# Kernel optimization log

Measured on AMD Instinct MI355X. Metric: run time of the kernel, lower is better.

The kernel has to match this reference:

```python
import jax, jax.numpy as jnp
import numpy as np

N = 50000      # nodes
E = 800000     # edges (before self-loops)
IN = 64        # in_dim
C = 64         # hidden_dim (per-head out channels)
H = 4          # heads
NEG_SLOPE = 0.2


def setup_inputs() -> dict:
    key = jax.random.key(0)
    ks = jax.random.split(key, 9)
    x = jax.random.normal(ks[0], (N, IN), jnp.float32)
    edge_index = jax.random.randint(ks[1], (2, E), 0, N)
    edge_attr = jax.random.uniform(ks[2], (E, 1), jnp.float32)
    s_in = 1.0 / np.sqrt(IN)
    s_c = 1.0 / np.sqrt(C)
    W = jax.random.normal(ks[3], (IN, H * C), jnp.float32) * s_in
    att_src = jax.random.normal(ks[4], (H, C), jnp.float32) * s_c
    att_dst = jax.random.normal(ks[5], (H, C), jnp.float32) * s_c
    lin_edge_w = jax.random.normal(ks[6], (1, H * C), jnp.float32)
    att_edge = jax.random.normal(ks[7], (H, C), jnp.float32) * s_c
    bias = jnp.zeros((C,), jnp.float32)
    return dict(x=x, edge_index=edge_index, edge_attr=edge_attr, W=W,
                att_src=att_src, att_dst=att_dst, lin_edge_w=lin_edge_w,
                att_edge=att_edge, bias=bias)


def reference(x, edge_index, edge_attr, W, att_src, att_dst, lin_edge_w, att_edge, bias):
    n = x.shape[0]
    # add self-loops (PyG default add_self_loops=True, fill_value='mean')
    loop = jnp.arange(n)
    src = jnp.concatenate([edge_index[0], loop])          # [E+N]
    dst = jnp.concatenate([edge_index[1], loop])          # [E+N]
    ea = jnp.concatenate([edge_attr,
                          jnp.full((n, 1), edge_attr.mean(), edge_attr.dtype)], axis=0)
    # node transform: [N, H, C]
    h = (x @ W).reshape(n, H, C)
    a_src = jnp.einsum('nhc,hc->nh', h, att_src)          # [N, H]
    a_dst = jnp.einsum('nhc,hc->nh', h, att_dst)          # [N, H]
    eh = (ea @ lin_edge_w).reshape(-1, H, C)              # [E+N, H, C]
    a_edge = jnp.einsum('ehc,hc->eh', eh, att_edge)       # [E+N, H]
    # per-edge attention logit
    alpha = a_src[src] + a_dst[dst] + a_edge              # [E+N, H]
    alpha = jax.nn.leaky_relu(alpha, NEG_SLOPE)
    # segment softmax over edges grouped by destination node
    amax = jax.ops.segment_max(alpha, dst, num_segments=n)
    alpha = jnp.exp(alpha - amax[dst])
    asum = jax.ops.segment_sum(alpha, dst, num_segments=n)
    alpha = alpha / (asum[dst] + 1e-16)                   # [E+N, H]
    # weighted message + scatter-add aggregation
    msg = h[src] * alpha[..., None]                       # [E+N, H, C]
    out = jax.ops.segment_sum(msg, dst, num_segments=n)   # [N, H, C]
    out = out.mean(axis=1) + bias                         # concat=False -> head mean
    # ReLU + residual
    return jax.nn.relu(out) + x
```

## Files before the change

### kernel.cpp

```cpp
#include <hip/hip_runtime.h>
#include <hip/hip_fp16.h>
#include <math.h>

#define H 4
#define C 64
#define HC 256
#define NEG 0.2f
#define BKT 128
#define BSH 7
#define TILE 2048
#define CSEG 32
#define MAXCR 31
#define MAXREC 63
#define XPAD 72
#define G1 512
#define NBMAX 392

typedef __attribute__((ext_vector_type(8))) _Float16 half8;
typedef __attribute__((ext_vector_type(4))) float f32x4;
typedef float f32x2 __attribute__((vector_size(8)));

__global__ __launch_bounds__(256) void phase1_kernel(
    const float* __restrict__ x, const float* __restrict__ W,
    const float* __restrict__ att_src, const float* __restrict__ att_dst,
    const int* __restrict__ ei, const float* __restrict__ edge_attr,
    unsigned char* __restrict__ h, float* __restrict__ a_src, float* __restrict__ a_dst,
    unsigned* __restrict__ arena, float* __restrict__ mean_acc,
    int Nn, int Ee, int ntile, int nbkt) {
    __shared__ __align__(16) char smem[NBMAX * CSEG * 4 + 1024];
    int t = threadIdx.x;
    if ((int)blockIdx.x < G1) {
        _Float16* xs = (_Float16*)smem;
        int w = t >> 6, lane = t & 63, quad = lane >> 4, c16 = lane & 15;
        half8 bf[4][2];
#pragma unroll
        for (int nt = 0; nt < 4; ++nt)
#pragma unroll
            for (int kh = 0; kh < 2; ++kh)
#pragma unroll
                for (int j = 0; j < 8; ++j)
                    bf[nt][kh][j] = (_Float16)W[(kh * 32 + quad * 8 + j) * HC +
                                                w * 64 + nt * 16 + c16];
        float ats[4], atd[4];
#pragma unroll
        for (int nt = 0; nt < 4; ++nt) {
            ats[nt] = att_src[w * 64 + nt * 16 + c16];
            atd[nt] = att_dst[w * 64 + nt * 16 + c16];
        }
        unsigned* h32 = (unsigned*)h;

        int nT = (Nn + 15) >> 4;
        for (int mt = blockIdx.x; mt < nT; mt += G1) {
            __syncthreads();
            {
                int row = t >> 4, col4 = (t & 15) * 4;
                int node = mt * 16 + row;
                float4 v = make_float4(0.f, 0.f, 0.f, 0.f);
                if (node < Nn) v = *(const float4*)(x + (size_t)node * 64 + col4);
                _Float16* dst = xs + row * XPAD + col4;
                dst[0] = (_Float16)v.x; dst[1] = (_Float16)v.y;
                dst[2] = (_Float16)v.z; dst[3] = (_Float16)v.w;
            }
            __syncthreads();
            half8 a0 = *(const half8*)(xs + c16 * XPAD + quad * 8);
            half8 a1 = *(const half8*)(xs + c16 * XPAD + 32 + quad * 8);
            f32x4 d[4];
#pragma unroll
            for (int nt = 0; nt < 4; ++nt) {
                f32x4 acc = {0.f, 0.f, 0.f, 0.f};
                acc = __builtin_amdgcn_mfma_f32_16x16x32_f16(a0, bf[nt][0], acc, 0, 0, 0);
                acc = __builtin_amdgcn_mfma_f32_16x16x32_f16(a1, bf[nt][1], acc, 0, 0, 0);
                d[nt] = acc;
            }
#pragma unroll
            for (int reg = 0; reg < 4; ++reg) {
                int node = mt * 16 + quad * 4 + reg;
                float ps = 0.f, pd = 0.f;
#pragma unroll
                for (int nt = 0; nt < 4; ++nt) {
                    ps += d[nt][reg] * ats[nt];
                    pd += d[nt][reg] * atd[nt];
                }
                ps += __shfl_xor(ps, 1); pd += __shfl_xor(pd, 1);
                ps += __shfl_xor(ps, 2); pd += __shfl_xor(pd, 2);
                ps += __shfl_xor(ps, 4); pd += __shfl_xor(pd, 4);
                ps += __shfl_xor(ps, 8); pd += __shfl_xor(pd, 8);
                if (node < Nn) {
                    if (c16 == 0) {
                        a_src[node * 4 + w] = ps;
                        a_dst[node * 4 + w] = pd;
                    }
                    int v = __builtin_amdgcn_cvt_pk_fp8_f32(d[0][reg], d[1][reg], 0, false);
                    v = __builtin_amdgcn_cvt_pk_fp8_f32(d[2][reg], d[3][reg], v, true);
                    h32[(size_t)node * 64 + w * 16 + c16] = (unsigned)v;
                }
            }
        }
    } else {
        unsigned* img = (unsigned*)smem;
        float* red = (float*)(smem + NBMAX * CSEG * 4);
        int tile = (int)blockIdx.x - G1;
        for (int c = t; c < nbkt; c += 256) img[c * CSEG] = 0;
        __syncthreads();
        int e0 = tile * TILE;
        float s = 0.f;
#pragma unroll 4
        for (int k = 0; k < TILE / 256; ++k) {
            int i = e0 + k * 256 + t;
            if (i < Ee) {
                int src = ei[i];
                int dst = ei[Ee + i];
                float ea = edge_attr[i];
                s += ea;
                unsigned q = (unsigned)(ea * 511.f + 0.5f);
                int b = dst >> BSH;
                unsigned r = atomicAdd(&img[b * CSEG], 1u);
                if (r < MAXCR)
                    img[b * CSEG + 1 + r] =
                        ((unsigned)src << 16) | (q << 7) | (unsigned)(dst & (BKT - 1));
            }
        }
        __syncthreads();
        for (int j = t; j < nbkt * CSEG; j += 256) {
            unsigned v = img[j];
            if ((j & (CSEG - 1)) == 0) v = v < (unsigned)MAXCR ? v : (unsigned)MAXCR;
            arena[((size_t)(j >> 5) * ntile + tile) * CSEG + (j & (CSEG - 1))] = v;
        }
        red[t] = s;
        __syncthreads();
        for (int o = 128; o; o >>= 1) {
            if (t < o) red[t] += red[t + o];
            __syncthreads();
        }
        if (t == 0) atomicAdd(mean_acc, red[0]);
    }
}

__global__ __launch_bounds__(512) void aggregate_kernel(
    const unsigned* __restrict__ arena,
    const float* __restrict__ a_src, const float* __restrict__ a_dst,
    const float* __restrict__ lin_edge_w, const float* __restrict__ att_edge,
    const float* __restrict__ mean_acc, const unsigned char* __restrict__ h,
    const float* __restrict__ bias, const float* __restrict__ x,
    float* __restrict__ out, int Nn, int ntile, float invE) {
    __shared__ unsigned rows[BKT * 64 + 64];
    __shared__ unsigned rcnt[BKT];
    __shared__ unsigned short cellc[NBMAX];
    int t = threadIdx.x;
    int b = blockIdx.x;
    int lane = t & 63, w = t >> 6;

    if (t < BKT) rcnt[t] = 0;
    size_t base = (size_t)b * ntile * CSEG;
    for (int c = t; c < ntile; c += 512) {
        unsigned v = arena[base + (size_t)c * CSEG];
        cellc[c] = (unsigned short)(v < (unsigned)MAXCR ? v : (unsigned)MAXCR);
    }
    __syncthreads();
    int tot = ntile * CSEG;
    for (int j = t; j < tot; j += 512) {
        int slot = j & (CSEG - 1);
        if (slot >= 1 && slot <= (int)cellc[j >> 5]) {
            unsigned rec = arena[base + j];
            unsigned dl = rec & 127u;
            unsigned r = atomicAdd(&rcnt[dl], 1u);
            if (r < MAXREC) rows[dl * 64 + 1 + r] = rec;
        }
    }
    __syncthreads();
    if (t < BKT) rows[t * 64] = rcnt[t] < (unsigned)MAXREC ? rcnt[t] : (unsigned)MAXREC;
    __syncthreads();

    int head = lane >> 4, sub = lane & 15;
    float kp = 0.f;
#pragma unroll
    for (int j = 0; j < 4; ++j) {
        int c = sub * 4 + j;
        kp += lin_edge_w[head * C + c] * att_edge[head * C + c];
    }
    kp += __shfl_xor(kp, 1);
    kp += __shfl_xor(kp, 2);
    kp += __shfl_xor(kp, 4);
    kp += __shfl_xor(kp, 8);
    float K = kp;
    float mean = mean_acc[0] * invE;
    const unsigned* h8 = (const unsigned*)h;
    const float DEQ = 1.0f / 511.f;
    int hb = lane & 48;

    for (int i = 0; i < BKT / 8; ++i) {
        int nl = w * (BKT / 8) + i;
        int n = b * BKT + nl;
        if (n >= Nn) break;
        unsigned deg = rows[nl * 64];
        unsigned rec = rows[nl * 64 + 1 + lane];
        unsigned sv = h8[(size_t)n * 64 + lane];
        float ad = a_dst[n * 4 + head];
        float asn = a_src[n * 4 + head];

        float wk0, wk1, wk2, wk3;
        {
            float wtmp[4];
#pragma unroll
            for (int k2 = 0; k2 < 4; ++k2) {
                int e = sub + 16 * k2;
                unsigned re = (unsigned)__shfl((int)rec, e);
                int se = (e < (int)deg) ? (int)(re >> 16) : 0;
                float lg = a_src[se * 4 + head] + ad +
                           (float)((re >> 7) & 511u) * DEQ * K;
                lg = lg > 0.f ? lg : NEG * lg;
                wtmp[k2] = (e < (int)deg) ? __expf(lg) : 0.f;
            }
            wk0 = wtmp[0]; wk1 = wtmp[1]; wk2 = wtmp[2]; wk3 = wtmp[3];
        }
        float sw = (wk0 + wk1) + (wk2 + wk3);
        sw += __shfl_xor(sw, 1);
        sw += __shfl_xor(sw, 2);
        sw += __shfl_xor(sw, 4);
        sw += __shfl_xor(sw, 8);

        float ls = asn + ad + mean * K;
        ls = ls > 0.f ? ls : NEG * ls;
        float wsl = __expf(ls);
        f32x2 s01 = __builtin_amdgcn_cvt_pk_f32_fp8((int)sv, false);
        f32x2 s23 = __builtin_amdgcn_cvt_pk_f32_fp8((int)sv, true);
        float4 acc = make_float4(wsl * s01[0], wsl * s01[1], wsl * s23[0], wsl * s23[1]);
        float swgt = sw + wsl;

        for (int g = 0; g < (int)deg; g += 8) {
            int cnt = (int)deg - g;
            if (cnt > 8) cnt = 8;
            unsigned hv0 = 0, hv1 = 0, hv2 = 0, hv3 = 0,
                     hv4 = 0, hv5 = 0, hv6 = 0, hv7 = 0;
#define GATH(u, dst)                                                          \
            if (u < cnt) {                                                    \
                unsigned r = (unsigned)__builtin_amdgcn_readlane((int)rec, g + u); \
                dst = h8[(size_t)(r >> 16) * 64 + lane];                      \
            }
            GATH(0, hv0) GATH(1, hv1) GATH(2, hv2) GATH(3, hv3)
            GATH(4, hv4) GATH(5, hv5) GATH(6, hv6) GATH(7, hv7)
#undef GATH
#define CONS(u, src)                                                          \
            if (u < cnt) {                                                    \
                int e = g + u;                                                \
                int k2 = e >> 4;                                              \
                float wsrc = (k2 == 0) ? wk0 : (k2 == 1) ? wk1                \
                             : (k2 == 2) ? wk2 : wk3;                         \
                float wg = __shfl(wsrc, hb | (e & 15));                       \
                f32x2 f01 = __builtin_amdgcn_cvt_pk_f32_fp8((int)src, false); \
                f32x2 f23 = __builtin_amdgcn_cvt_pk_f32_fp8((int)src, true);  \
                acc.x += wg * f01[0]; acc.y += wg * f01[1];                   \
                acc.z += wg * f23[0]; acc.w += wg * f23[1];                   \
            }
            CONS(0, hv0) CONS(1, hv1) CONS(2, hv2) CONS(3, hv3)
            CONS(4, hv4) CONS(5, hv5) CONS(6, hv6) CONS(7, hv7)
#undef CONS
        }

        float inv = 1.f / (swgt + 1e-16f);
        acc.x *= inv; acc.y *= inv; acc.z *= inv; acc.w *= inv;

        acc.x += __shfl_xor(acc.x, 16);
        acc.y += __shfl_xor(acc.y, 16);
        acc.z += __shfl_xor(acc.z, 16);
        acc.w += __shfl_xor(acc.w, 16);
        acc.x += __shfl_xor(acc.x, 32);
        acc.y += __shfl_xor(acc.y, 32);
        acc.z += __shfl_xor(acc.z, 32);
        acc.w += __shfl_xor(acc.w, 32);
        if (lane < 16) {
            float b0 = bias[lane], b1 = bias[16 + lane];
            float b2 = bias[32 + lane], b3 = bias[48 + lane];
            const float* xr = x + (size_t)n * 64 + lane;
            float x0 = xr[0], x1 = xr[16], x2 = xr[32], x3 = xr[48];
            float* orow = out + (size_t)n * 64 + lane;
            orow[0]  = fmaxf(acc.x * 0.25f + b0, 0.f) + x0;
            orow[16] = fmaxf(acc.y * 0.25f + b1, 0.f) + x1;
            orow[32] = fmaxf(acc.z * 0.25f + b2, 0.f) + x2;
            orow[48] = fmaxf(acc.w * 0.25f + b3, 0.f) + x3;
        }
    }
}

extern "C" void kernel_launch(void* const* d_in, const int* in_sizes, int n_in,
                              void* d_out, int out_size, void* d_ws, size_t ws_size,
                              hipStream_t stream) {
    const float* x = (const float*)d_in[0];
    const int* ei = (const int*)d_in[1];
    const float* edge_attr = (const float*)d_in[2];
    const float* W = (const float*)d_in[3];
    const float* att_src = (const float*)d_in[4];
    const float* att_dst = (const float*)d_in[5];
    const float* lin_edge_w = (const float*)d_in[6];
    const float* att_edge = (const float*)d_in[7];
    const float* bias = (const float*)d_in[8];
    float* out = (float*)d_out;
    int Nn = in_sizes[0] / 64;
    int Ee = in_sizes[1] / 2;
    int nbkt = (Nn + BKT - 1) >> BSH;
    int ntile = (Ee + TILE - 1) / TILE;

    char* p = (char*)d_ws;
    size_t off = 0;
    auto alloc = [&](size_t bytes) -> char* {
        char* r = p + off;
        off += (bytes + 255) & ~(size_t)255;
        return r;
    };
    float* mean_acc = (float*)alloc(256);
    size_t zero_bytes = off;
    unsigned* arena = (unsigned*)alloc((size_t)nbkt * ntile * CSEG * 4);
    unsigned char* h = (unsigned char*)alloc((size_t)Nn * HC);
    float* a_src = (float*)alloc((size_t)Nn * H * 4);
    float* a_dst = (float*)alloc((size_t)Nn * H * 4);
    (void)ws_size;

    hipMemsetAsync(d_ws, 0, zero_bytes, stream);
    phase1_kernel<<<G1 + ntile, 256, 0, stream>>>(x, W, att_src, att_dst,
                                                  ei, edge_attr, h, a_src, a_dst,
                                                  arena, mean_acc,
                                                  Nn, Ee, ntile, nbkt);
    aggregate_kernel<<<nbkt, 512, 0, stream>>>(arena, a_src, a_dst,
                                               lin_edge_w, att_edge, mean_acc,
                                               h, bias, x, out, Nn, ntile,
                                               1.0f / (float)Ee);
}
```

Baseline: 175.4 us.

## Split bucket compaction from aggregation into separate per-node-wave kernel

Splits the fused aggregate kernel into two. A bucket kernel compacts arena records into per-node rows in global memory, and a new aggregate kernel assigns one wave per node across many small blocks. The aim is finer-grained parallelism and better latency hiding than the old layout, where a 512-thread block per 128-node bucket looped over 16 nodes per wave behind a large shared-memory footprint. In exchange it adds an extra launch and a global round trip for the compacted edge rows.

```diff
diff --git a/kernel.cpp b/kernel.cpp
--- a/kernel.cpp
+++ b/kernel.cpp
@@ -136,29 +136,22 @@
     }
 }
 
-__global__ __launch_bounds__(512) void aggregate_kernel(
-    const unsigned* __restrict__ arena,
-    const float* __restrict__ a_src, const float* __restrict__ a_dst,
-    const float* __restrict__ lin_edge_w, const float* __restrict__ att_edge,
-    const float* __restrict__ mean_acc, const unsigned char* __restrict__ h,
-    const float* __restrict__ bias, const float* __restrict__ x,
-    float* __restrict__ out, int Nn, int ntile, float invE) {
-    __shared__ unsigned rows[BKT * 64 + 64];
+__global__ __launch_bounds__(256) void bucket_kernel(
+    const unsigned* __restrict__ arena, unsigned* __restrict__ edges,
+    int ntile, int nbkt) {
+    __shared__ unsigned rows[BKT * 64];
     __shared__ unsigned rcnt[BKT];
     __shared__ unsigned short cellc[NBMAX];
-    int t = threadIdx.x;
-    int b = blockIdx.x;
-    int lane = t & 63, w = t >> 6;
-
+    int b = blockIdx.x, t = threadIdx.x;
     if (t < BKT) rcnt[t] = 0;
     size_t base = (size_t)b * ntile * CSEG;
-    for (int c = t; c < ntile; c += 512) {
+    for (int c = t; c < ntile; c += 256) {
         unsigned v = arena[base + (size_t)c * CSEG];
         cellc[c] = (unsigned short)(v < (unsigned)MAXCR ? v : (unsigned)MAXCR);
     }
     __syncthreads();
     int tot = ntile * CSEG;
-    for (int j = t; j < tot; j += 512) {
+    for (int j = t; j < tot; j += 256) {
         int slot = j & (CSEG - 1);
         if (slot >= 1 && slot <= (int)cellc[j >> 5]) {
             unsigned rec = arena[base + j];
@@ -170,8 +163,33 @@
     __syncthreads();
     if (t < BKT) rows[t * 64] = rcnt[t] < (unsigned)MAXREC ? rcnt[t] : (unsigned)MAXREC;
     __syncthreads();
-
-    int head = lane >> 4, sub = lane & 15;
+    size_t obase = (size_t)b * (BKT * 64);
+    for (int i = t; i < BKT * 16; i += 256)
+        *(uint4*)(edges + obase + i * 4) = *(const uint4*)(rows + i * 4);
+}
+
+__global__ __launch_bounds__(256) void aggregate_kernel(
+    const unsigned* __restrict__ edges,
+    const float* __restrict__ a_src, const float* __restrict__ a_dst,
+    const float* __restrict__ lin_edge_w, const float* __restrict__ att_edge,
+    const float* __restrict__ mean_acc, const unsigned char* __restrict__ h,
+    const float* __restrict__ bias, const float* __restrict__ x,
+    float* __restrict__ out, int Nn, float invE) {
+    int lane = threadIdx.x & 63;
+    int n = blockIdx.x * 4 + (threadIdx.x >> 6);
+    if (n >= Nn) return;
+    int head = lane >> 4;
+    int sub = lane & 15;
+
+    size_t rowbase = (size_t)n * 64;
+    unsigned deg = edges[rowbase];
+    unsigned rec = edges[rowbase + 1 + lane];
+    const unsigned* h8 = (const unsigned*)h;
+    unsigned sv = h8[(size_t)n * 64 + lane];
+    float mean = mean_acc[0] * invE;
+    float ad = a_dst[n * 4 + head];
+    float asn = a_src[n * 4 + head];
+
     float kp = 0.f;
 #pragma unroll
     for (int j = 0; j < 4; ++j) {
@@ -183,102 +201,88 @@
     kp += __shfl_xor(kp, 4);
     kp += __shfl_xor(kp, 8);
     float K = kp;
-    float mean = mean_acc[0] * invE;
-    const unsigned* h8 = (const unsigned*)h;
     const float DEQ = 1.0f / 511.f;
+
+    if (deg > MAXREC) deg = MAXREC;
+
+    float wk0, wk1, wk2, wk3;
+    {
+        float wtmp[4];
+#pragma unroll
+        for (int k = 0; k < 4; ++k) {
+            int e = sub + 16 * k;
+            unsigned re = (unsigned)__shfl((int)rec, e);
+            int se = (e < (int)deg) ? (int)(re >> 16) : 0;
+            float lg = a_src[se * 4 + head] + ad + (float)((re >> 7) & 511u) * DEQ * K;
+            lg = lg > 0.f ? lg : NEG * lg;
+            wtmp[k] = (e < (int)deg) ? __expf(lg) : 0.f;
+        }
+        wk0 = wtmp[0]; wk1 = wtmp[1]; wk2 = wtmp[2]; wk3 = wtmp[3];
+    }
+    float sw = (wk0 + wk1) + (wk2 + wk3);
+    sw += __shfl_xor(sw, 1);
+    sw += __shfl_xor(sw, 2);
+    sw += __shfl_xor(sw, 4);
+    sw += __shfl_xor(sw, 8);
+
+    float ls = asn + ad + mean * K;
+    ls = ls > 0.f ? ls : NEG * ls;
+    float wsl = __expf(ls);
+    f32x2 s01 = __builtin_amdgcn_cvt_pk_f32_fp8((int)sv, false);
+    f32x2 s23 = __builtin_amdgcn_cvt_pk_f32_fp8((int)sv, true);
+    float4 acc = make_float4(wsl * s01[0], wsl * s01[1], wsl * s23[0], wsl * s23[1]);
+    float swgt = sw + wsl;
     int hb = lane & 48;
 
-    for (int i = 0; i < BKT / 8; ++i) {
-        int nl = w * (BKT / 8) + i;
-        int n = b * BKT + nl;
-        if (n >= Nn) break;
-        unsigned deg = rows[nl * 64];
-        unsigned rec = rows[nl * 64 + 1 + lane];
-        unsigned sv = h8[(size_t)n * 64 + lane];
-        float ad = a_dst[n * 4 + head];
-        float asn = a_src[n * 4 + head];
-
-        float wk0, wk1, wk2, wk3;
-        {
-            float wtmp[4];
-#pragma unroll
-            for (int k2 = 0; k2 < 4; ++k2) {
-                int e = sub + 16 * k2;
-                unsigned re = (unsigned)__shfl((int)rec, e);
-                int se = (e < (int)deg) ? (int)(re >> 16) : 0;
-                float lg = a_src[se * 4 + head] + ad +
-                           (float)((re >> 7) & 511u) * DEQ * K;
-                lg = lg > 0.f ? lg : NEG * lg;
-                wtmp[k2] = (e < (int)deg) ? __expf(lg) : 0.f;
-            }
-            wk0 = wtmp[0]; wk1 = wtmp[1]; wk2 = wtmp[2]; wk3 = wtmp[3];
-        }
-        float sw = (wk0 + wk1) + (wk2 + wk3);
-        sw += __shfl_xor(sw, 1);
-        sw += __shfl_xor(sw, 2);
-        sw += __shfl_xor(sw, 4);
-        sw += __shfl_xor(sw, 8);
-
-        float ls = asn + ad + mean * K;
-        ls = ls > 0.f ? ls : NEG * ls;
-        float wsl = __expf(ls);
-        f32x2 s01 = __builtin_amdgcn_cvt_pk_f32_fp8((int)sv, false);
-        f32x2 s23 = __builtin_amdgcn_cvt_pk_f32_fp8((int)sv, true);
-        float4 acc = make_float4(wsl * s01[0], wsl * s01[1], wsl * s23[0], wsl * s23[1]);
-        float swgt = sw + wsl;
-
-        for (int g = 0; g < (int)deg; g += 8) {
-            int cnt = (int)deg - g;
-            if (cnt > 8) cnt = 8;
-            unsigned hv0 = 0, hv1 = 0, hv2 = 0, hv3 = 0,
-                     hv4 = 0, hv5 = 0, hv6 = 0, hv7 = 0;
+    for (int g = 0; g < (int)deg; g += 8) {
+        int cnt = (int)deg - g;
+        if (cnt > 8) cnt = 8;
+        unsigned hv0 = 0, hv1 = 0, hv2 = 0, hv3 = 0, hv4 = 0, hv5 = 0, hv6 = 0, hv7 = 0;
 #define GATH(u, dst)                                                          \
-            if (u < cnt) {                                                    \
-                unsigned r = (unsigned)__builtin_amdgcn_readlane((int)rec, g + u); \
-                dst = h8[(size_t)(r >> 16) * 64 + lane];                      \
-            }
-            GATH(0, hv0) GATH(1, hv1) GATH(2, hv2) GATH(3, hv3)
-            GATH(4, hv4) GATH(5, hv5) GATH(6, hv6) GATH(7, hv7)
+        if (u < cnt) {                                                        \
+            unsigned r = (unsigned)__builtin_amdgcn_readlane((int)rec, g + u);\
+            dst = h8[(size_t)(r >> 16) * 64 + lane];                          \
+        }
+        GATH(0, hv0) GATH(1, hv1) GATH(2, hv2) GATH(3, hv3)
+        GATH(4, hv4) GATH(5, hv5) GATH(6, hv6) GATH(7, hv7)
 #undef GATH
 #define CONS(u, src)                                                          \
-            if (u < cnt) {                                                    \
-                int e = g + u;                                                \
-                int k2 = e >> 4;                                              \
-                float wsrc = (k2 == 0) ? wk0 : (k2 == 1) ? wk1                \
-                             : (k2 == 2) ? wk2 : wk3;                         \
-                float wg = __shfl(wsrc, hb | (e & 15));                       \
-                f32x2 f01 = __builtin_amdgcn_cvt_pk_f32_fp8((int)src, false); \
-                f32x2 f23 = __builtin_amdgcn_cvt_pk_f32_fp8((int)src, true);  \
-                acc.x += wg * f01[0]; acc.y += wg * f01[1];                   \
-                acc.z += wg * f23[0]; acc.w += wg * f23[1];                   \
-            }
-            CONS(0, hv0) CONS(1, hv1) CONS(2, hv2) CONS(3, hv3)
-            CONS(4, hv4) CONS(5, hv5) CONS(6, hv6) CONS(7, hv7)
+        if (u < cnt) {                                                        \
+            int e = g + u;                                                    \
+            int k = e >> 4;                                                   \
+            float wsrc = (k == 0) ? wk0 : (k == 1) ? wk1 : (k == 2) ? wk2 : wk3; \
+            float wg = __shfl(wsrc, hb | (e & 15));                           \
+            f32x2 f01 = __builtin_amdgcn_cvt_pk_f32_fp8((int)src, false);     \
+            f32x2 f23 = __builtin_amdgcn_cvt_pk_f32_fp8((int)src, true);      \
+            acc.x += wg * f01[0]; acc.y += wg * f01[1];                       \
+            acc.z += wg * f23[0]; acc.w += wg * f23[1];                       \
+        }
+        CONS(0, hv0) CONS(1, hv1) CONS(2, hv2) CONS(3, hv3)
+        CONS(4, hv4) CONS(5, hv5) CONS(6, hv6) CONS(7, hv7)
 #undef CONS
-        }
-
-        float inv = 1.f / (swgt + 1e-16f);
-        acc.x *= inv; acc.y *= inv; acc.z *= inv; acc.w *= inv;
-
-        acc.x += __shfl_xor(acc.x, 16);
-        acc.y += __shfl_xor(acc.y, 16);
-        acc.z += __shfl_xor(acc.z, 16);
-        acc.w += __shfl_xor(acc.w, 16);
-        acc.x += __shfl_xor(acc.x, 32);
-        acc.y += __shfl_xor(acc.y, 32);
-        acc.z += __shfl_xor(acc.z, 32);
-        acc.w += __shfl_xor(acc.w, 32);
-        if (lane < 16) {
-            float b0 = bias[lane], b1 = bias[16 + lane];
-            float b2 = bias[32 + lane], b3 = bias[48 + lane];
-            const float* xr = x + (size_t)n * 64 + lane;
-            float x0 = xr[0], x1 = xr[16], x2 = xr[32], x3 = xr[48];
-            float* orow = out + (size_t)n * 64 + lane;
-            orow[0]  = fmaxf(acc.x * 0.25f + b0, 0.f) + x0;
-            orow[16] = fmaxf(acc.y * 0.25f + b1, 0.f) + x1;
-            orow[32] = fmaxf(acc.z * 0.25f + b2, 0.f) + x2;
-            orow[48] = fmaxf(acc.w * 0.25f + b3, 0.f) + x3;
-        }
+    }
+
+    float inv = 1.f / (swgt + 1e-16f);
+    acc.x *= inv; acc.y *= inv; acc.z *= inv; acc.w *= inv;
+
+    acc.x += __shfl_xor(acc.x, 16);
+    acc.y += __shfl_xor(acc.y, 16);
+    acc.z += __shfl_xor(acc.z, 16);
+    acc.w += __shfl_xor(acc.w, 16);
+    acc.x += __shfl_xor(acc.x, 32);
+    acc.y += __shfl_xor(acc.y, 32);
+    acc.z += __shfl_xor(acc.z, 32);
+    acc.w += __shfl_xor(acc.w, 32);
+    if (lane < 16) {
+        float b0 = bias[lane], b1 = bias[16 + lane];
+        float b2 = bias[32 + lane], b3 = bias[48 + lane];
+        const float* xr = x + (size_t)n * 64 + lane;
+        float x0 = xr[0], x1 = xr[16], x2 = xr[32], x3 = xr[48];
+        float* orow = out + (size_t)n * 64 + lane;
+        orow[0]  = fmaxf(acc.x * 0.25f + b0, 0.f) + x0;
+        orow[16] = fmaxf(acc.y * 0.25f + b1, 0.f) + x1;
+        orow[32] = fmaxf(acc.z * 0.25f + b2, 0.f) + x2;
+        orow[48] = fmaxf(acc.w * 0.25f + b3, 0.f) + x3;
     }
 }
 
@@ -310,6 +314,7 @@
     float* mean_acc = (float*)alloc(256);
     size_t zero_bytes = off;
     unsigned* arena = (unsigned*)alloc((size_t)nbkt * ntile * CSEG * 4);
+    unsigned* edges = (unsigned*)alloc((size_t)nbkt * BKT * 64 * 4);
     unsigned char* h = (unsigned char*)alloc((size_t)Nn * HC);
     float* a_src = (float*)alloc((size_t)Nn * H * 4);
     float* a_dst = (float*)alloc((size_t)Nn * H * 4);
@@ -320,8 +325,9 @@
                                                   ei, edge_attr, h, a_src, a_dst,
                                                   arena, mean_acc,
                                                   Nn, Ee, ntile, nbkt);
-    aggregate_kernel<<<nbkt, 512, 0, stream>>>(arena, a_src, a_dst,
-                                               lin_edge_w, att_edge, mean_acc,
-                                               h, bias, x, out, Nn, ntile,
-                                               1.0f / (float)Ee);
+    bucket_kernel<<<nbkt, 256, 0, stream>>>(arena, edges, ntile, nbkt);
+    aggregate_kernel<<<(Nn + 3) / 4, 256, 0, stream>>>(edges, a_src, a_dst,
+                                                       lin_edge_w, att_edge, mean_acc,
+                                                       h, bias, x, out, Nn,
+                                                       1.0f / (float)Ee);
 }
```

Result: faster. 157.5 us (-10.2%).
